# Optimization experiments

Measured on AMD Instinct MI355X. Metric: run time of the kernel, lower is better.

The kernel has to match this reference:

```python
import jax, jax.numpy as jnp
import numpy as np

H = 768      # hidden_size
NH = 12      # num_heads
HD = H // NH # head_size
MLP = 3072
B, N = 16, 577


def setup_inputs() -> dict:
    key = jax.random.key(0)
    ks = jax.random.split(key, 16)
    s = 0.02
    return {
        "x": jax.random.normal(ks[0], (B, N, H), jnp.float32),
        "Wq": jax.random.normal(ks[1], (H, H), jnp.float32) * s,
        "bq": jnp.zeros((H,), jnp.float32),
        "Wk": jax.random.normal(ks[2], (H, H), jnp.float32) * s,
        "bk": jnp.zeros((H,), jnp.float32),
        "Wv": jax.random.normal(ks[3], (H, H), jnp.float32) * s,
        "bv": jnp.zeros((H,), jnp.float32),
        "Wo": jax.random.normal(ks[4], (H, H), jnp.float32) * s,
        "bo": jnp.zeros((H,), jnp.float32),
        "W1": jax.random.normal(ks[5], (H, MLP), jnp.float32) * s,
        "b1": jnp.zeros((MLP,), jnp.float32),
        "W2": jax.random.normal(ks[6], (MLP, H), jnp.float32) * s,
        "b2": jnp.zeros((H,), jnp.float32),
        "ln1_g": jnp.ones((H,), jnp.float32),
        "ln1_b": jnp.zeros((H,), jnp.float32),
        "ln2_g": jnp.ones((H,), jnp.float32),
        "ln2_b": jnp.zeros((H,), jnp.float32),
    }


def _layernorm(x, g, b, eps=1e-6):
    mu = jnp.mean(x, axis=-1, keepdims=True)
    var = jnp.mean(jnp.square(x - mu), axis=-1, keepdims=True)
    return (x - mu) * jax.lax.rsqrt(var + eps) * g + b


def reference(x, Wq, bq, Wk, bk, Wv, bv, Wo, bo, W1, b1, W2, b2,
              ln1_g, ln1_b, ln2_g, ln2_b):
    h = x
    y = _layernorm(x, ln1_g, ln1_b)
    # projections [B,N,H] -> [B,NH,N,HD]
    def heads(t):
        return t.reshape(B, N, NH, HD).transpose(0, 2, 1, 3)
    q = heads(y @ Wq + bq)
    _k = heads(y @ Wk + bk)  # computed but UNUSED (bug in original: Q@V^T)
    v = heads(y @ Wv + bv)
    # faithful to source: scores = Q @ V^T (not K)
    scores = jnp.einsum('bhqd,bhkd->bhqk', q, v) / jnp.sqrt(jnp.float32(HD))
    probs = jax.nn.softmax(scores, axis=-1)
    o = jnp.einsum('bhqk,bhkd->bhqd', probs, v)
    o = o.transpose(0, 2, 1, 3).reshape(B, N, H)
    attn_out = o @ Wo + bo
    x1 = attn_out + h
    h2 = x1
    y2 = _layernorm(x1, ln2_g, ln2_b)
    m = jax.nn.gelu(y2 @ W1 + b1, approximate=False)
    m = m @ W2 + b2
    return m + h2
```

## Files before the change

kernel.cpp:

```cpp
#include <hip/hip_runtime.h>


#define GLOBAL_AS __attribute__((address_space(1)))
#define LDS_AS __attribute__((address_space(3)))

typedef __bf16 bf16x8 __attribute__((ext_vector_type(8)));
typedef float f32x4 __attribute__((ext_vector_type(4)));
typedef unsigned short u16x8 __attribute__((ext_vector_type(8)));

static __device__ __forceinline__ f32x4 mfma16(bf16x8 a, bf16x8 b, f32x4 c) {
  return __builtin_amdgcn_mfma_f32_16x16x32_bf16(a, b, c, 0, 0, 0);
}

static __device__ __forceinline__ unsigned short f2bf(float f) {
  union { float f; unsigned u; } v; v.f = f;
  unsigned r = v.u + 0x7fffu + ((v.u >> 16) & 1u);
  return (unsigned short)(r >> 16);
}

static __device__ __forceinline__ void async16(const void* g, void* l) {
  __builtin_amdgcn_global_load_lds((const GLOBAL_AS void*)g, (LDS_AS void*)l, 16, 0, 0);
}

static __device__ __forceinline__ float gelu_exact(float x) {
  return 0.5f * x * (1.0f + erff(x * 0.70710678118654752f));
}

static __device__ __forceinline__ void tc_body(const float* __restrict__ W,
                                               unsigned short* __restrict__ Wt,
                                               int K, int ldw, int nb, int kb,
                                               int t) {
  __shared__ float tile[32][33];
  const int tr = t >> 5, tc = t & 31;
#pragma unroll
  for (int p = 0; p < 4; ++p)
    tile[p * 8 + tr][tc] = W[(size_t)(kb + p * 8 + tr) * ldw + nb + tc];
  __syncthreads();
#pragma unroll
  for (int p = 0; p < 4; ++p)
    Wt[(size_t)(nb + p * 8 + tr) * K + kb + tc] = f2bf(tile[tc][p * 8 + tr]);
}

__global__ __launch_bounds__(256)
void transpose_cast(const float* __restrict__ W, unsigned short* __restrict__ Wt,
                    int K, int ldw) {
  tc_body(W, Wt, K, ldw, blockIdx.x * 32, blockIdx.y * 32, threadIdx.x);
}

__global__ __launch_bounds__(256)
void transpose_qv(const float* __restrict__ Wq, const float* __restrict__ Wv,
                  unsigned short* __restrict__ Wt) {
  const float* W = blockIdx.z ? Wv : Wq;
  unsigned short* dst = Wt + (size_t)blockIdx.z * 768 * 768;
  tc_body(W, dst, 768, 768, blockIdx.x * 32, blockIdx.y * 32, threadIdx.x);
}

__global__ __launch_bounds__(256)
void transpose_mlp(const float* __restrict__ W1, const float* __restrict__ W2,
                   unsigned short* __restrict__ W1Ts,
                   unsigned short* __restrict__ W2Ts, int s) {
  int id = blockIdx.x;
  if (id < 1152) {
    const int bx = id % 48, by = id / 48;
    tc_body(W1 + s * 1536, W1Ts, 768, 3072, bx * 32, by * 32, threadIdx.x);
  } else {
    id -= 1152;
    const int bx = id % 24, by = id / 24;
    tc_body(W2 + (size_t)s * 1536 * 768, W2Ts, 1536, 768, bx * 32, by * 32,
            threadIdx.x);
  }
}

__global__ __launch_bounds__(256)
void ln_f32(const float* __restrict__ x, const float* __restrict__ g,
            const float* __restrict__ be, unsigned short* __restrict__ y) {
  const int w = threadIdx.x >> 6, lane = threadIdx.x & 63;
  const size_t row = (size_t)blockIdx.x * 4 + w;
  const float* xr = x + row * 768;
  float vv[12];
#pragma unroll
  for (int j = 0; j < 3; ++j) {
    float4 v = *(const float4*)(xr + j * 256 + lane * 4);
    vv[j * 4 + 0] = v.x; vv[j * 4 + 1] = v.y;
    vv[j * 4 + 2] = v.z; vv[j * 4 + 3] = v.w;
  }
  float s = 0.f;
#pragma unroll
  for (int j = 0; j < 12; ++j) s += vv[j];
#pragma unroll
  for (int o = 32; o > 0; o >>= 1) s += __shfl_xor(s, o);
  const float mu = s * (1.0f / 768.0f);
  float q = 0.f;
#pragma unroll
  for (int j = 0; j < 12; ++j) { float d = vv[j] - mu; q += d * d; }
#pragma unroll
  for (int o = 32; o > 0; o >>= 1) q += __shfl_xor(q, o);
  const float rstd = rsqrtf(q * (1.0f / 768.0f) + 1e-6f);
  unsigned short* yr = y + row * 768;
#pragma unroll
  for (int j = 0; j < 3; ++j) {
    float4 gv = *(const float4*)(g + j * 256 + lane * 4);
    float4 bv = *(const float4*)(be + j * 256 + lane * 4);
    ushort4 o4;
    o4.x = f2bf((vv[j * 4 + 0] - mu) * rstd * gv.x + bv.x);
    o4.y = f2bf((vv[j * 4 + 1] - mu) * rstd * gv.y + bv.y);
    o4.z = f2bf((vv[j * 4 + 2] - mu) * rstd * gv.z + bv.z);
    o4.w = f2bf((vv[j * 4 + 3] - mu) * rstd * gv.w + bv.w);
    *(ushort4*)(yr + j * 256 + lane * 4) = o4;
  }
}

template <int ACT, int RES, int OUTF32, int NB, int SPLIT>
__global__ __launch_bounds__(256, 2)
void gemm_bt(const unsigned short* __restrict__ A,
             const unsigned short* __restrict__ B,
             const float* __restrict__ bias,
             const float* __restrict__ bias2,
             const float* __restrict__ resid,
             void* __restrict__ out1, void* __restrict__ out2,
             int M, int N, int K) {
  __shared__ __align__(16) unsigned short As[2][128 * 32];
  __shared__ __align__(16) unsigned short Bs[2][128 * 32];
  const int t = threadIdx.x;
  const int m0 = blockIdx.x * 128;
  const int n0 = blockIdx.y * 128;
  const int w = t >> 6, lane = t & 63;
  const int lr = lane & 15, lg = lane >> 4;
  const int wrr = (w >> 1) * 64, wcc = (w & 1) * 64;
  f32x4 acc[4][4] = {};

  auto stage = [&](int buf, int k0) {
#pragma unroll
    for (int p = 0; p < 2; ++p) {
      int i = p * 256 + t;
      int row = i >> 2, c = (i & 3) << 3;
      int ar = m0 + row; ar = ar < M ? ar : M - 1;
      async16(A + (size_t)ar * K + k0 + c, &As[buf][i * 8]);
      async16(B + (size_t)(n0 + row) * K + k0 + c, &Bs[buf][i * 8]);
    }
  };

  stage(0, 0);
  __syncthreads();
  int cur = 0;
  for (int k0 = 0; k0 < K; k0 += 32) {
    if (k0 + 32 < K) stage(cur ^ 1, k0 + 32);
    bf16x8 af[4], bfr[4];
#pragma unroll
    for (int mi = 0; mi < 4; ++mi)
      af[mi] = *(const bf16x8*)(&As[cur][(wrr + mi * 16 + lr) * 32 + lg * 8]);
#pragma unroll
    for (int ni = 0; ni < 4; ++ni)
      bfr[ni] = *(const bf16x8*)(&Bs[cur][(wcc + ni * 16 + lr) * 32 + lg * 8]);
#pragma unroll
    for (int mi = 0; mi < 4; ++mi)
#pragma unroll
      for (int ni = 0; ni < 4; ++ni)
        acc[mi][ni] = mfma16(af[mi], bfr[ni], acc[mi][ni]);
    __syncthreads();
    cur ^= 1;
  }
  const int orow = m0 + wrr + lg * 4;
  const int ocol = n0 + wcc + lr;
#pragma unroll
  for (int mi = 0; mi < 4; ++mi) {
#pragma unroll
    for (int ni = 0; ni < 4; ++ni) {
      const int col = ocol + ni * 16;
      float bs;
      if (SPLIT)
        bs = (col < 768) ? bias[col] : bias2[col - 768];
      else
        bs = NB ? 0.f : bias[col];
      f32x4 a = acc[mi][ni];
#pragma unroll
      for (int r = 0; r < 4; ++r) {
        const int row = orow + mi * 16 + r;
        if (row < M) {
          float v = a[r] + bs;
          if (ACT == 1) v = gelu_exact(v);
          if (RES == 1) v += resid[(size_t)row * N + col];
          if (SPLIT) {
            if (col < 768)
              ((unsigned short*)out1)[(size_t)row * 768 + col] = f2bf(v);
            else
              ((unsigned short*)out2)[(size_t)row * 768 + col - 768] = f2bf(v);
          } else if (OUTF32) {
            ((float*)out1)[(size_t)row * N + col] = v;
          } else {
            ((unsigned short*)out1)[(size_t)row * N + col] = f2bf(v);
          }
        }
      }
    }
  }
}

__global__ __launch_bounds__(256, 2)
void attn_fused(const unsigned short* __restrict__ Q,
                const unsigned short* __restrict__ V,
                unsigned short* __restrict__ O) {
  __shared__ __align__(16) unsigned short Vn[64 * 72];
  __shared__ __align__(16) unsigned short Vt[64 * 72];
  __shared__ __align__(16) unsigned short Pl[4][32 * 72];
  const int qt = blockIdx.x, h = blockIdx.y, b = blockIdx.z;
  const int t = threadIdx.x, w = t >> 6, lane = t & 63;
  const int lr = lane & 15, lg = lane >> 4;
  const int q0 = qt * 128 + w * 32;
  bf16x8 aq[2][2];
#pragma unroll
  for (int mi = 0; mi < 2; ++mi) {
    int qrow = q0 + mi * 16 + lr; qrow = qrow < 577 ? qrow : 576;
    const unsigned short* qp = Q + ((size_t)(b * 577 + qrow)) * 768 + h * 64;
    aq[mi][0] = *(const bf16x8*)(qp + lg * 8);
    aq[mi][1] = *(const bf16x8*)(qp + 32 + lg * 8);
  }
  bf16x8 ones;
#pragma unroll
  for (int j = 0; j < 8; ++j) ones[j] = (__bf16)1.0f;
  f32x4 oacc[2][4] = {};
  f32x4 lac[2] = {};
  const unsigned short* vp = V + (size_t)b * 577 * 768 + h * 64;

  for (int kt = 0; kt < 10; ++kt) {
    const int k0 = kt * 64;
#pragma unroll
    for (int p = 0; p < 2; ++p) {
      int i = p * 256 + t;
      int kr = i >> 3, c = (i & 7) << 3;
      int gk = k0 + kr; gk = gk < 577 ? gk : 576;
      bf16x8 vv = *(const bf16x8*)(vp + (size_t)gk * 768 + c);
      *(bf16x8*)(Vn + kr * 72 + c) = vv;
    }
    __syncthreads();
#pragma unroll
    for (int p = 0; p < 2; ++p) {
      int i = p * 256 + t;
      int d = i & 63, kb = (i >> 6) * 8;
      u16x8 tv;
#pragma unroll
      for (int j = 0; j < 8; ++j) tv[j] = Vn[(kb + j) * 72 + d];
      *(u16x8*)(Vt + d * 72 + kb) = tv;
    }
    f32x4 s[2][4];
#pragma unroll
    for (int mi = 0; mi < 2; ++mi)
#pragma unroll
      for (int ni = 0; ni < 4; ++ni) {
        f32x4 a = {};
        a = mfma16(aq[mi][0], *(const bf16x8*)(Vn + (ni * 16 + lr) * 72 + lg * 8), a);
        a = mfma16(aq[mi][1], *(const bf16x8*)(Vn + (ni * 16 + lr) * 72 + 32 + lg * 8), a);
        s[mi][ni] = a * 0.125f;
      }
    if (kt == 9) {
#pragma unroll
      for (int ni = 0; ni < 4; ++ni) {
        int kc = k0 + ni * 16 + lr;
        if (kc >= 577) {
#pragma unroll
          for (int mi = 0; mi < 2; ++mi) {
            s[mi][ni][0] = -1e30f; s[mi][ni][1] = -1e30f;
            s[mi][ni][2] = -1e30f; s[mi][ni][3] = -1e30f;
          }
        }
      }
    }
#pragma unroll
    for (int mi = 0; mi < 2; ++mi)
#pragma unroll
      for (int ni = 0; ni < 4; ++ni)
#pragma unroll
        for (int r = 0; r < 4; ++r)
          Pl[w][(mi * 16 + lg * 4 + r) * 72 + ni * 16 + lr] =
              f2bf(__expf(s[mi][ni][r]));
    __syncthreads();
#pragma unroll
    for (int mi = 0; mi < 2; ++mi) {
      const bf16x8 pa0 = *(const bf16x8*)(&Pl[w][(mi * 16 + lr) * 72 + lg * 8]);
      const bf16x8 pa1 = *(const bf16x8*)(&Pl[w][(mi * 16 + lr) * 72 + 32 + lg * 8]);
#pragma unroll
      for (int di = 0; di < 4; ++di) {
        oacc[mi][di] = mfma16(pa0, *(const bf16x8*)(Vt + (di * 16 + lr) * 72 + lg * 8), oacc[mi][di]);
        oacc[mi][di] = mfma16(pa1, *(const bf16x8*)(Vt + (di * 16 + lr) * 72 + 32 + lg * 8), oacc[mi][di]);
      }
      lac[mi] = mfma16(pa0, ones, lac[mi]);
      lac[mi] = mfma16(pa1, ones, lac[mi]);
    }
  }
#pragma unroll
  for (int mi = 0; mi < 2; ++mi)
#pragma unroll
    for (int r = 0; r < 4; ++r) {
      const int qg = q0 + mi * 16 + lg * 4 + r;
      if (qg < 577) {
        const float inv = 1.0f / lac[mi][r];
        unsigned short* op = O + ((size_t)(b * 577 + qg)) * 768 + h * 64 + lr;
#pragma unroll
        for (int di = 0; di < 4; ++di) op[di * 16] = f2bf(oacc[mi][di][r] * inv);
      }
    }
}

extern "C" void kernel_launch(void* const* d_in, const int* in_sizes, int n_in,
                              void* d_out, int out_size, void* d_ws, size_t ws_size,
                              hipStream_t stream) {
  (void)in_sizes; (void)n_in; (void)out_size; (void)ws_size;
  const float* x   = (const float*)d_in[0];
  const float* Wq  = (const float*)d_in[1];
  const float* bq  = (const float*)d_in[2];
  const float* Wv  = (const float*)d_in[5];
  const float* bv  = (const float*)d_in[6];
  const float* Wo  = (const float*)d_in[7];
  const float* bo  = (const float*)d_in[8];
  const float* W1  = (const float*)d_in[9];
  const float* b1  = (const float*)d_in[10];
  const float* W2  = (const float*)d_in[11];
  const float* b2  = (const float*)d_in[12];
  const float* g1  = (const float*)d_in[13];
  const float* be1 = (const float*)d_in[14];
  const float* g2  = (const float*)d_in[15];
  const float* be2 = (const float*)d_in[16];
  float* out = (float*)d_out;

  const size_t BF = (size_t)9232 * 768 * 2;
  char* ws = (char*)d_ws;
  unsigned short* sA = (unsigned short*)(ws);
  unsigned short* sB = (unsigned short*)(ws + BF);
  unsigned short* sC = (unsigned short*)(ws + 2 * BF);
  unsigned short* sD = (unsigned short*)(ws + 3 * BF);
  unsigned short* mb = sC;

  dim3 blk(256);

  ln_f32<<<dim3(2308), blk, 0, stream>>>(x, g1, be1, sA);
  transpose_qv<<<dim3(24, 24, 2), blk, 0, stream>>>(Wq, Wv, sD);
  gemm_bt<0, 0, 0, 0, 1><<<dim3(73, 12), blk, 0, stream>>>(
      sA, sD, bq, bv, nullptr, sB, sC, 9232, 1536, 768);

  attn_fused<<<dim3(5, 12, 16), blk, 0, stream>>>(sB, sC, sA);

  transpose_cast<<<dim3(24, 24), blk, 0, stream>>>(Wo, sD, 768, 768);
  gemm_bt<0, 1, 1, 0, 0><<<dim3(73, 6), blk, 0, stream>>>(
      sA, sD, bo, nullptr, x, out, nullptr, 9232, 768, 768);

  ln_f32<<<dim3(2308), blk, 0, stream>>>(out, g2, be2, sB);

  for (int s = 0; s < 2; ++s) {
    unsigned short* W1Ts = sA;
    unsigned short* W2Ts = sA + 1536 * 768;
    transpose_mlp<<<dim3(2304), blk, 0, stream>>>(W1, W2, W1Ts, W2Ts, s);
    gemm_bt<1, 0, 0, 0, 0><<<dim3(73, 12), blk, 0, stream>>>(
        sB, W1Ts, b1 + s * 1536, nullptr, nullptr, mb, nullptr, 9232, 1536, 768);
    if (s == 0) {
      gemm_bt<0, 1, 1, 0, 0><<<dim3(73, 6), blk, 0, stream>>>(
          mb, W2Ts, b2, nullptr, out, out, nullptr, 9232, 768, 1536);
    } else {
      gemm_bt<0, 1, 1, 1, 0><<<dim3(73, 6), blk, 0, stream>>>(
          mb, W2Ts, nullptr, nullptr, out, out, nullptr, 9232, 768, 1536);
    }
  }
}
```

Before: 377.1 us.

## Remap GEMM workgroups per XCD, use finer waitcnt pipelining, hoist MLP weight transposes

The GEMM kernel now runs on a 1D grid and remaps block IDs so consecutive tiles land on the same XCD, with N-tiles fastest, to improve L2 reuse of the shared A row-panel. The K-loop replaces __syncthreads with explicit vmcnt/lgkmcnt waits and raw barriers, so the prefetch of the next tile stays in flight while the current tile computes. Both MLP weight-slice transposes are launched up front into separate workspace regions rather than inside the loop. The hand-written waitcnt counts assume exactly four outstanding loads per stage, so they depend on the stage layout staying as it is.

Result: faster. 347.7 us (-7.8%).

```diff
diff --git a/kernel.cpp b/kernel.cpp
--- a/kernel.cpp
+++ b/kernel.cpp
@@ -122,8 +122,13 @@
   __shared__ __align__(16) unsigned short As[2][128 * 32];
   __shared__ __align__(16) unsigned short Bs[2][128 * 32];
   const int t = threadIdx.x;
-  const int m0 = blockIdx.x * 128;
-  const int n0 = blockIdx.y * 128;
+  const int nwg = gridDim.x;
+  const int q8 = nwg >> 3, r8 = nwg & 7;
+  const int xcd = blockIdx.x & 7, jj = blockIdx.x >> 3;
+  const int wgid = (xcd < r8 ? xcd * (q8 + 1) : r8 * (q8 + 1) + (xcd - r8) * q8) + jj;
+  const int gn = N >> 7;
+  const int m0 = (wgid / gn) * 128;
+  const int n0 = (wgid % gn) * 128;
   const int w = t >> 6, lane = t & 63;
   const int lr = lane & 15, lg = lane >> 4;
   const int wrr = (w >> 1) * 64, wcc = (w & 1) * 64;
@@ -141,10 +146,16 @@
   };
 
   stage(0, 0);
-  __syncthreads();
   int cur = 0;
-  for (int k0 = 0; k0 < K; k0 += 32) {
-    if (k0 + 32 < K) stage(cur ^ 1, k0 + 32);
+  const int nt = K >> 5;
+  for (int tt = 0; tt < nt; ++tt) {
+    if (tt + 1 < nt) {
+      stage(cur ^ 1, (tt + 1) << 5);
+      asm volatile("s_waitcnt vmcnt(4)" ::: "memory");
+    } else {
+      asm volatile("s_waitcnt vmcnt(0)" ::: "memory");
+    }
+    __builtin_amdgcn_s_barrier();
     bf16x8 af[4], bfr[4];
 #pragma unroll
     for (int mi = 0; mi < 4; ++mi)
@@ -152,12 +163,14 @@
 #pragma unroll
     for (int ni = 0; ni < 4; ++ni)
       bfr[ni] = *(const bf16x8*)(&Bs[cur][(wcc + ni * 16 + lr) * 32 + lg * 8]);
+    asm volatile("s_waitcnt lgkmcnt(0)" ::: "memory");
+    __builtin_amdgcn_sched_barrier(0);
+    __builtin_amdgcn_s_barrier();
 #pragma unroll
     for (int mi = 0; mi < 4; ++mi)
 #pragma unroll
       for (int ni = 0; ni < 4; ++ni)
         acc[mi][ni] = mfma16(af[mi], bfr[ni], acc[mi][ni]);
-    __syncthreads();
     cur ^= 1;
   }
   const int orow = m0 + wrr + lg * 4;
@@ -329,33 +342,36 @@
   unsigned short* sC = (unsigned short*)(ws + 2 * BF);
   unsigned short* sD = (unsigned short*)(ws + 3 * BF);
   unsigned short* mb = sC;
+  const size_t WSL = (size_t)1536 * 768;
 
   dim3 blk(256);
 
   ln_f32<<<dim3(2308), blk, 0, stream>>>(x, g1, be1, sA);
   transpose_qv<<<dim3(24, 24, 2), blk, 0, stream>>>(Wq, Wv, sD);
-  gemm_bt<0, 0, 0, 0, 1><<<dim3(73, 12), blk, 0, stream>>>(
+  gemm_bt<0, 0, 0, 0, 1><<<dim3(876), blk, 0, stream>>>(
       sA, sD, bq, bv, nullptr, sB, sC, 9232, 1536, 768);
 
   attn_fused<<<dim3(5, 12, 16), blk, 0, stream>>>(sB, sC, sA);
 
   transpose_cast<<<dim3(24, 24), blk, 0, stream>>>(Wo, sD, 768, 768);
-  gemm_bt<0, 1, 1, 0, 0><<<dim3(73, 6), blk, 0, stream>>>(
+  gemm_bt<0, 1, 1, 0, 0><<<dim3(438), blk, 0, stream>>>(
       sA, sD, bo, nullptr, x, out, nullptr, 9232, 768, 768);
 
   ln_f32<<<dim3(2308), blk, 0, stream>>>(out, g2, be2, sB);
 
+  transpose_mlp<<<dim3(2304), blk, 0, stream>>>(W1, W2, sA, sA + WSL, 0);
+  transpose_mlp<<<dim3(2304), blk, 0, stream>>>(W1, W2, sA + 2 * WSL, sA + 3 * WSL, 1);
+
   for (int s = 0; s < 2; ++s) {
-    unsigned short* W1Ts = sA;
-    unsigned short* W2Ts = sA + 1536 * 768;
-    transpose_mlp<<<dim3(2304), blk, 0, stream>>>(W1, W2, W1Ts, W2Ts, s);
-    gemm_bt<1, 0, 0, 0, 0><<<dim3(73, 12), blk, 0, stream>>>(
+    unsigned short* W1Ts = sA + (size_t)(2 * s) * WSL;
+    unsigned short* W2Ts = sA + (size_t)(2 * s + 1) * WSL;
+    gemm_bt<1, 0, 0, 0, 0><<<dim3(876), blk, 0, stream>>>(
         sB, W1Ts, b1 + s * 1536, nullptr, nullptr, mb, nullptr, 9232, 1536, 768);
     if (s == 0) {
-      gemm_bt<0, 1, 1, 0, 0><<<dim3(73, 6), blk, 0, stream>>>(
+      gemm_bt<0, 1, 1, 0, 0><<<dim3(438), blk, 0, stream>>>(
           mb, W2Ts, b2, nullptr, out, out, nullptr, 9232, 768, 1536);
     } else {
-      gemm_bt<0, 1, 1, 1, 0><<<dim3(73, 6), blk, 0, stream>>>(
+      gemm_bt<0, 1, 1, 1, 0><<<dim3(438), blk, 0, stream>>>(
           mb, W2Ts, nullptr, nullptr, out, out, nullptr, 9232, 768, 1536);
     }
   }
```
